# Kernel optimization log

Hardware: AMD Instinct MI355X
Metric: run time of the kernel (lower is better)

Reference implementation:

```python
import jax, jax.numpy as jnp
import numpy as np

B, IN, HS = 4096, 1024, 1024


def setup_inputs() -> dict:
    key = jax.random.key(0)
    ks = jax.random.split(key, 20)
    inp = {
        "x": jax.random.normal(ks[0], (B, IN), jnp.float32),
        "h": jax.random.normal(ks[1], (B, HS), jnp.float32),
        "c": jax.random.normal(ks[2], (B, HS), jnp.float32),
    }
    names_x = ["Wix", "Wfx", "Wgx", "Wox"]
    names_h = ["Wih", "Wfh", "Wgh", "Woh"]
    bnames_x = ["bix", "bfx", "bgx", "box"]
    bnames_h = ["bih", "bfh", "bgh", "boh"]
    k = 3
    for wn, bn in zip(names_x, bnames_x):
        inp[wn] = jax.random.normal(ks[k], (HS, IN), jnp.float32) * 0.02; k += 1
        inp[bn] = jax.random.normal(ks[k], (HS,), jnp.float32) * 0.02; k += 1
    for wn, bn in zip(names_h, bnames_h):
        inp[wn] = jax.random.normal(ks[k], (HS, HS), jnp.float32) * 0.02; k += 1
        inp[bn] = jax.random.normal(ks[k], (HS,), jnp.float32) * 0.02; k += 1
    return inp


def reference(x, h, c,
              Wix, bix, Wfx, bfx, Wgx, bgx, Wox, box,
              Wih, bih, Wfh, bfh, Wgh, bgh, Woh, boh):
    # torch Linear: y = x @ W.T + b
    i = jax.nn.sigmoid(x @ Wix.T + bix + h @ Wih.T + bih)
    f = jax.nn.sigmoid(x @ Wfx.T + bfx + h @ Wfh.T + bfh)
    g = jnp.tanh(x @ Wgx.T + bgx + h @ Wgh.T + bgh)
    o = jax.nn.sigmoid(x @ Wox.T + box + h @ Woh.T + boh)
    c_new = f * c + i * g
    h_new = o * jnp.tanh(c_new)
    return (h_new, c_new)
```

## Files before the change

kernel.cpp:

```cpp
#include <hip/hip_runtime.h>
#include <hip/hip_bf16.h>
#include <stdint.h>

#define BATCH  4096
#define IN_DIM 1024
#define HS     1024
#define K_DIM  2048
#define N_DIM  4096
#define BK 64
#define NKT (K_DIM / BK)
#define HALF_BYTES 16384
#define TPB_BYTES  (NKT * HALF_BYTES)

typedef __bf16 bf16x8 __attribute__((ext_vector_type(8)));
typedef float  f32x4  __attribute__((ext_vector_type(4)));

__device__ __forceinline__ unsigned short f2bf(float f) {
    union { float f; uint32_t u; } a; a.f = f;
    uint32_t r = a.u + 0x7FFF + ((a.u >> 16) & 1);
    return (unsigned short)(r >> 16);
}
__device__ __forceinline__ uint32_t pk2(float a, float b) {
    return (uint32_t)f2bf(a) | ((uint32_t)f2bf(b) << 16);
}

__device__ __forceinline__ void load16_lds(const void* g, void* l) {
    __builtin_amdgcn_global_load_lds(
        (const __attribute__((address_space(1))) uint32_t*)g,
        (__attribute__((address_space(3))) uint32_t*)(uintptr_t)l,
        16, 0, 0);
}
__device__ __forceinline__ void stage16k(const char* g, char* l, int wid, int lane) {
    load16_lds(g + wid * 1024 + lane * 16,        l + wid * 1024);
    load16_lds(g + 8192 + wid * 1024 + lane * 16, l + 8192 + wid * 1024);
}

__device__ __forceinline__ float sigf(float x)  { return 1.0f / (1.0f + __expf(-x)); }
__device__ __forceinline__ float tanhf_(float x){ return 1.0f - 2.0f / (__expf(2.0f * x) + 1.0f); }

#define BAR()   __builtin_amdgcn_s_barrier()
#define DSB()   __builtin_amdgcn_sched_barrier(0)
#define PRIO(x) __builtin_amdgcn_s_setprio(x)

__device__ __forceinline__ void rdA(bf16x8 (&d)[4], const char* base, int kb) {
    #pragma unroll
    for (int i = 0; i < 4; ++i) d[i] = *(const bf16x8*)(base + i * 2048 + kb);
}
__device__ __forceinline__ void rdB(bf16x8 (&d)[4], const char* base, int kb) {
    #pragma unroll
    for (int i = 0; i < 4; ++i) d[i] = *(const bf16x8*)(base + i * 2048 + kb);
}
__device__ __forceinline__ void mfma16(f32x4 (&acc)[8][4], int mh,
                                       const bf16x8 (&a)[4], const bf16x8 (&b)[4]) {
    #pragma unroll
    for (int i = 0; i < 4; ++i)
        #pragma unroll
        for (int j = 0; j < 4; ++j)
            acc[mh * 4 + i][j] = __builtin_amdgcn_mfma_f32_16x16x32_bf16(
                a[i], b[j], acc[mh * 4 + i][j], 0, 0, 0);
}

__global__ void pack_kernel(const float* __restrict__ x, const float* __restrict__ h,
                            const float* __restrict__ Wix, const float* __restrict__ Wfx,
                            const float* __restrict__ Wgx, const float* __restrict__ Wox,
                            const float* __restrict__ Wih, const float* __restrict__ Wfh,
                            const float* __restrict__ Wgh, const float* __restrict__ Woh,
                            uint4* __restrict__ Apk, uint4* __restrict__ Bpk)
{
    int t = blockIdx.x * blockDim.x + threadIdx.x;
    const int NCHUNK = (BATCH * K_DIM) / 8;
    bool isB = t >= NCHUNK;
    int ci = isB ? (t - NCHUNK) : t;

    int cb  = ci & 7;
    int row = (ci >> 3) & 127;
    int kt  = (ci >> 10) & 31;
    int bt  = ci >> 15;

    int k0 = kt * BK + ((cb ^ (row & 7)) << 3);
    int gr = bt * 128 + row;

    const float* src;
    if (!isB) {
        src = (k0 < IN_DIM) ? (x + (size_t)gr * IN_DIM + k0)
                            : (h + (size_t)gr * HS + (k0 - IN_DIM));
    } else {
        int q = (gr >> 4) & 3;
        int u = ((gr >> 6) << 4) | (gr & 15);
        const float* Wq = (k0 < IN_DIM)
            ? ((q == 0) ? Wix : (q == 1) ? Wfx : (q == 2) ? Wgx : Wox)
            : ((q == 0) ? Wih : (q == 1) ? Wfh : (q == 2) ? Wgh : Woh);
        int kk = (k0 < IN_DIM) ? k0 : (k0 - IN_DIM);
        src = Wq + (size_t)u * 1024 + kk;
    }
    float4 v0 = ((const float4*)src)[0];
    float4 v1 = ((const float4*)src)[1];
    uint4 o;
    o.x = pk2(v0.x, v0.y); o.y = pk2(v0.z, v0.w);
    o.z = pk2(v1.x, v1.y); o.w = pk2(v1.z, v1.w);
    (isB ? Bpk : Apk)[ci] = o;
}

__global__ void __launch_bounds__(512, 2)
gemm_kernel(const char* __restrict__ Apk, const char* __restrict__ Bpk,
            const float* __restrict__ c,
            const float* __restrict__ bix, const float* __restrict__ bfx,
            const float* __restrict__ bgx, const float* __restrict__ box_,
            const float* __restrict__ bih, const float* __restrict__ bfh,
            const float* __restrict__ bgh, const float* __restrict__ boh,
            float* __restrict__ out)
{
    __shared__ uint4 lds4[131072 / 16];
    char* lds = (char*)lds4;

    const int tid  = threadIdx.x;
    const int lane = tid & 63;
    const int wid  = tid >> 6;
    const int wm   = wid >> 2;
    const int wn   = wid & 3;
    const int fr   = lane & 15;
    const int kg   = lane >> 4;

    const int phys = blockIdx.x;
    const int virt = (phys & 7) * 32 + (phys >> 3);
    const int bn   = virt & 15;
    const int bm   = virt >> 4;

    const char* gA = Apk + (size_t)(bm * 2) * TPB_BYTES;
    const char* gB = Bpk + (size_t)(bn * 2) * TPB_BYTES;

    const int sw  = (fr & 7) << 4;
    const int kb0 = (kg * 16) ^ sw;
    const int kb1 = (64 + kg * 16) ^ sw;
    const int aB  = wm * HALF_BYTES + fr * 128;
    const int bB  = 32768 + (wn >> 1) * HALF_BYTES + ((wn & 1) * 64 + fr) * 128;

    f32x4 acc[8][4] = {};

    stage16k(gA + (size_t)(0 * NKT + 0) * HALF_BYTES, lds + 0,     wid, lane);
    stage16k(gA + (size_t)(1 * NKT + 0) * HALF_BYTES, lds + 16384, wid, lane);
    stage16k(gB + (size_t)(0 * NKT + 0) * HALF_BYTES, lds + 32768, wid, lane);
    stage16k(gB + (size_t)(1 * NKT + 0) * HALF_BYTES, lds + 49152, wid, lane);
    stage16k(gB + (size_t)(0 * NKT + 1) * HALF_BYTES, lds + 65536 + 32768, wid, lane);
    stage16k(gB + (size_t)(1 * NKT + 1) * HALF_BYTES, lds + 65536 + 49152, wid, lane);
    asm volatile("s_waitcnt vmcnt(4)" ::: "memory");
    BAR(); DSB();

    for (int kt = 0; kt < NKT; ++kt) {
        char* L  = lds + (kt & 1) * 65536;
        char* Ln = lds + ((kt & 1) ^ 1) * 65536;
        const bool s1 = (kt + 1 < NKT), s2 = (kt + 2 < NKT);
        bf16x8 aX[4], aY[4], b0[4], b1[4];

        rdA(aX, L + aB, kb0);
        rdB(b0, L + bB, kb0);
        if (s1) stage16k(gA + (size_t)(0 * NKT + kt + 1) * HALF_BYTES, Ln + 0, wid, lane);
        PRIO(1); mfma16(acc, 0, aX, b0); PRIO(0);
        BAR(); DSB();

        rdA(aY, L + aB, kb1);
        rdB(b1, L + bB, kb1);
        if (s1) stage16k(gA + (size_t)(1 * NKT + kt + 1) * HALF_BYTES, Ln + 16384, wid, lane);
        PRIO(1); mfma16(acc, 0, aY, b1); PRIO(0);
        BAR(); DSB();

        rdA(aX, L + aB + 8192, kb0);
        if (s2) stage16k(gB + (size_t)(0 * NKT + kt + 2) * HALF_BYTES, L + 32768, wid, lane);
        PRIO(1); mfma16(acc, 1, aX, b0); PRIO(0);
        BAR(); DSB();

        rdA(aY, L + aB + 8192, kb1);
        if (s2) stage16k(gB + (size_t)(1 * NKT + kt + 2) * HALF_BYTES, L + 49152, wid, lane);
        PRIO(1); mfma16(acc, 1, aY, b1); PRIO(0);
        if (kt < NKT - 2) asm volatile("s_waitcnt vmcnt(4)" ::: "memory");
        else              asm volatile("s_waitcnt vmcnt(0)" ::: "memory");
        BAR(); DSB();
    }

    const int u  = bn * 64 + wn * 16 + fr;
    const int r0 = bm * 256 + wm * 128;
    const float bi = bix[u] + bih[u];
    const float bf = bfx[u] + bfh[u];
    const float bg = bgx[u] + bgh[u];
    const float bo = box_[u] + boh[u];
    float* hout = out;
    float* cout = out + (size_t)BATCH * HS;

    #pragma unroll
    for (int ai = 0; ai < 8; ++ai) {
        const int rowb = r0 + ai * 16 + kg * 4;
        #pragma unroll
        for (int r = 0; r < 4; ++r) {
            const size_t idx = (size_t)(rowb + r) * HS + u;
            float iv = sigf  (acc[ai][0][r] + bi);
            float fv = sigf  (acc[ai][1][r] + bf);
            float gv = tanhf_(acc[ai][2][r] + bg);
            float ov = sigf  (acc[ai][3][r] + bo);
            float cn = fv * c[idx] + iv * gv;
            hout[idx] = ov * tanhf_(cn);
            cout[idx] = cn;
        }
    }
}

extern "C" void kernel_launch(void* const* d_in, const int* in_sizes, int n_in,
                              void* d_out, int out_size, void* d_ws, size_t ws_size,
                              hipStream_t stream)
{
    const float* x   = (const float*)d_in[0];
    const float* h   = (const float*)d_in[1];
    const float* c   = (const float*)d_in[2];
    const float* Wix = (const float*)d_in[3];  const float* bix = (const float*)d_in[4];
    const float* Wfx = (const float*)d_in[5];  const float* bfx = (const float*)d_in[6];
    const float* Wgx = (const float*)d_in[7];  const float* bgx = (const float*)d_in[8];
    const float* Wox = (const float*)d_in[9];  const float* box_ = (const float*)d_in[10];
    const float* Wih = (const float*)d_in[11]; const float* bih = (const float*)d_in[12];
    const float* Wfh = (const float*)d_in[13]; const float* bfh = (const float*)d_in[14];
    const float* Wgh = (const float*)d_in[15]; const float* bgh = (const float*)d_in[16];
    const float* Woh = (const float*)d_in[17]; const float* boh = (const float*)d_in[18];

    char* ws = (char*)d_ws;
    uint4* Apk = (uint4*)ws;
    uint4* Bpk = (uint4*)(ws + (size_t)16 * 1024 * 1024);

    pack_kernel<<<8192, 256, 0, stream>>>(x, h, Wix, Wfx, Wgx, Wox,
                                          Wih, Wfh, Wgh, Woh, Apk, Bpk);
    gemm_kernel<<<256, 512, 0, stream>>>((const char*)Apk, (const char*)Bpk, c,
                                         bix, bfx, bgx, box_, bih, bfh, bgh, boh,
                                         (float*)d_out);
}
```

Before: 84.34 us.

## Restructure GEMM main loop with register double-buffered fragments and deeper prefetch

Rewrites the K-loop of the fused LSTM GEMM so that B fragments are double-buffered in registers and A fragments are read one quarter-step ahead. Global-to-LDS staging for both A and B is now issued two tiles ahead, and the loop is unrolled by two with a single barrier per MFMA quarter. Scheduling barriers are removed and the waitcnt thresholds are retuned, so LDS read latency should overlap with MFMA work. The trade-offs are higher register pressure, a few wasted wrap-around prefetches at the end of the loop, and tighter LDS overwrite hazards that depend on the barrier placement being correct.

After: 83.51 us. Within noise of the previous version (-1.0%).

```diff
diff --git a/kernel.cpp b/kernel.cpp
--- a/kernel.cpp
+++ b/kernel.cpp
@@ -39,25 +39,32 @@
 __device__ __forceinline__ float tanhf_(float x){ return 1.0f - 2.0f / (__expf(2.0f * x) + 1.0f); }
 
 #define BAR()   __builtin_amdgcn_s_barrier()
-#define DSB()   __builtin_amdgcn_sched_barrier(0)
 #define PRIO(x) __builtin_amdgcn_s_setprio(x)
 
-__device__ __forceinline__ void rdA(bf16x8 (&d)[4], const char* base, int kb) {
+__device__ __forceinline__ void rdA4(bf16x8 (&d)[4], const char* base, int kb0, int kb1) {
+    d[0] = *(const bf16x8*)(base + kb0);
+    d[1] = *(const bf16x8*)(base + kb1);
+    d[2] = *(const bf16x8*)(base + 2048 + kb0);
+    d[3] = *(const bf16x8*)(base + 2048 + kb1);
+}
+__device__ __forceinline__ void rdB8(bf16x8 (&d)[8], const char* base, int kb0, int kb1) {
     #pragma unroll
-    for (int i = 0; i < 4; ++i) d[i] = *(const bf16x8*)(base + i * 2048 + kb);
-}
-__device__ __forceinline__ void rdB(bf16x8 (&d)[4], const char* base, int kb) {
+    for (int j = 0; j < 4; ++j) {
+        d[j]     = *(const bf16x8*)(base + j * 2048 + kb0);
+        d[4 + j] = *(const bf16x8*)(base + j * 2048 + kb1);
+    }
+}
+template<int Q>
+__device__ __forceinline__ void mfq(f32x4 (&acc)[8][4], const bf16x8 (&a)[4],
+                                    const bf16x8 (&b)[8]) {
     #pragma unroll
-    for (int i = 0; i < 4; ++i) d[i] = *(const bf16x8*)(base + i * 2048 + kb);
-}
-__device__ __forceinline__ void mfma16(f32x4 (&acc)[8][4], int mh,
-                                       const bf16x8 (&a)[4], const bf16x8 (&b)[4]) {
-    #pragma unroll
-    for (int i = 0; i < 4; ++i)
+    for (int mf = 0; mf < 2; ++mf)
         #pragma unroll
-        for (int j = 0; j < 4; ++j)
-            acc[mh * 4 + i][j] = __builtin_amdgcn_mfma_f32_16x16x32_bf16(
-                a[i], b[j], acc[mh * 4 + i][j], 0, 0, 0);
+        for (int ks = 0; ks < 2; ++ks)
+            #pragma unroll
+            for (int j = 0; j < 4; ++j)
+                acc[2 * Q + mf][j] = __builtin_amdgcn_mfma_f32_16x16x32_bf16(
+                    a[mf * 2 + ks], b[ks * 4 + j], acc[2 * Q + mf][j], 0, 0, 0);
 }
 
 __global__ void pack_kernel(const float* __restrict__ x, const float* __restrict__ h,
@@ -129,13 +136,13 @@
     const char* gA = Apk + (size_t)(bm * 2) * TPB_BYTES;
     const char* gB = Bpk + (size_t)(bn * 2) * TPB_BYTES;
 
-    const int sw  = (fr & 7) << 4;
-    const int kb0 = (kg * 16) ^ sw;
-    const int kb1 = (64 + kg * 16) ^ sw;
-    const int aB  = wm * HALF_BYTES + fr * 128;
-    const int bB  = 32768 + (wn >> 1) * HALF_BYTES + ((wn & 1) * 64 + fr) * 128;
+    const int kb0   = (kg * 16) ^ ((fr & 7) << 4);
+    const int kb1   = kb0 ^ 64;
+    const int aBase = wm * 16384 + fr * 128;
+    const int bBase = 32768 + wn * 8192 + fr * 128;
 
     f32x4 acc[8][4] = {};
+    bf16x8 aE[4], aO[4], bA_[8], bB_[8];
 
     stage16k(gA + (size_t)(0 * NKT + 0) * HALF_BYTES, lds + 0,     wid, lane);
     stage16k(gA + (size_t)(1 * NKT + 0) * HALF_BYTES, lds + 16384, wid, lane);
@@ -143,39 +150,42 @@
     stage16k(gB + (size_t)(1 * NKT + 0) * HALF_BYTES, lds + 49152, wid, lane);
     stage16k(gB + (size_t)(0 * NKT + 1) * HALF_BYTES, lds + 65536 + 32768, wid, lane);
     stage16k(gB + (size_t)(1 * NKT + 1) * HALF_BYTES, lds + 65536 + 49152, wid, lane);
-    asm volatile("s_waitcnt vmcnt(4)" ::: "memory");
-    BAR(); DSB();
-
-    for (int kt = 0; kt < NKT; ++kt) {
-        char* L  = lds + (kt & 1) * 65536;
-        char* Ln = lds + ((kt & 1) ^ 1) * 65536;
-        const bool s1 = (kt + 1 < NKT), s2 = (kt + 2 < NKT);
-        bf16x8 aX[4], aY[4], b0[4], b1[4];
-
-        rdA(aX, L + aB, kb0);
-        rdB(b0, L + bB, kb0);
-        if (s1) stage16k(gA + (size_t)(0 * NKT + kt + 1) * HALF_BYTES, Ln + 0, wid, lane);
-        PRIO(1); mfma16(acc, 0, aX, b0); PRIO(0);
-        BAR(); DSB();
-
-        rdA(aY, L + aB, kb1);
-        rdB(b1, L + bB, kb1);
-        if (s1) stage16k(gA + (size_t)(1 * NKT + kt + 1) * HALF_BYTES, Ln + 16384, wid, lane);
-        PRIO(1); mfma16(acc, 0, aY, b1); PRIO(0);
-        BAR(); DSB();
-
-        rdA(aX, L + aB + 8192, kb0);
-        if (s2) stage16k(gB + (size_t)(0 * NKT + kt + 2) * HALF_BYTES, L + 32768, wid, lane);
-        PRIO(1); mfma16(acc, 1, aX, b0); PRIO(0);
-        BAR(); DSB();
-
-        rdA(aY, L + aB + 8192, kb1);
-        if (s2) stage16k(gB + (size_t)(1 * NKT + kt + 2) * HALF_BYTES, L + 49152, wid, lane);
-        PRIO(1); mfma16(acc, 1, aY, b1); PRIO(0);
-        if (kt < NKT - 2) asm volatile("s_waitcnt vmcnt(4)" ::: "memory");
-        else              asm volatile("s_waitcnt vmcnt(0)" ::: "memory");
-        BAR(); DSB();
-    }
+    stage16k(gA + (size_t)(0 * NKT + 1) * HALF_BYTES, lds + 65536 + 0,     wid, lane);
+    stage16k(gA + (size_t)(1 * NKT + 1) * HALF_BYTES, lds + 65536 + 16384, wid, lane);
+    asm volatile("s_waitcnt vmcnt(8)" ::: "memory");
+    BAR();
+    rdB8(bA_, lds + bBase, kb0, kb1);
+    rdA4(aE, lds + aBase, kb0, kb1);
+
+#define TILE(L, LN, KT2, BCUR, BNXT)                                          \
+    {                                                                 \
+      asm volatile("s_waitcnt vmcnt(4)" ::: "memory");                        \
+      stage16k(gB + (size_t)(0 * NKT + (KT2)) * HALF_BYTES, (L) + 32768, wid, lane); \
+      rdA4(aO, (L) + aBase + 4096, kb0, kb1);                                 \
+      rdB8(BNXT, (LN) + bBase, kb0, kb1);                                     \
+      PRIO(1); mfq<0>(acc, aE, BCUR); PRIO(0); BAR();                         \
+                                                                      \
+      stage16k(gB + (size_t)(1 * NKT + (KT2)) * HALF_BYTES, (L) + 49152, wid, lane); \
+      rdA4(aE, (L) + aBase + 8192, kb0, kb1);                                 \
+      PRIO(1); mfq<1>(acc, aO, BCUR); PRIO(0); BAR();                         \
+                                                                      \
+      stage16k(gA + (size_t)(0 * NKT + (KT2)) * HALF_BYTES, (L) + 0, wid, lane); \
+      rdA4(aO, (L) + aBase + 12288, kb0, kb1);                                \
+      PRIO(1); mfq<2>(acc, aE, BCUR); PRIO(0); BAR();                         \
+                                                                      \
+      asm volatile("s_waitcnt vmcnt(6)" ::: "memory");                        \
+      stage16k(gA + (size_t)(1 * NKT + (KT2)) * HALF_BYTES, (L) + 16384, wid, lane); \
+      rdA4(aE, (LN) + aBase, kb0, kb1);                                       \
+      PRIO(1); mfq<3>(acc, aO, BCUR); PRIO(0); BAR();                         \
+    }
+
+    for (int it = 0; it < NKT / 2; ++it) {
+        const int k2e = (it * 2 + 2) & (NKT - 1);
+        const int k2o = (it * 2 + 3) & (NKT - 1);
+        TILE(lds,         lds + 65536, k2e, bA_, bB_);
+        TILE(lds + 65536, lds,         k2o, bB_, bA_);
+    }
+#undef TILE
 
     const int u  = bn * 64 + wn * 16 + fr;
     const int r0 = bm * 256 + wm * 128;
```

## Split waves into ping-pong groups with staggered LDS reads and MFMA phases

Applied to the files above, without the earlier changes.

The GEMM main loop is split by wave row: wm==0 waves read fragments then run MFMA right away, while wm==1 waves preload fragments one phase ahead, including the next k-tile's first fragments. Paired barriers offset the two groups so that one group's LDS reads and global-to-LDS staging overlap the other group's MFMA bursts. The intent is to hide LDS latency and keep the matrix cores busy. In exchange it doubles the barriers per phase and adds register pressure from prefetched fragments, and the barrier counts of the two groups must match exactly.

Result: no change. 84.38 us (+0.0%).

```diff
diff --git a/kernel.cpp b/kernel.cpp
--- a/kernel.cpp
+++ b/kernel.cpp
@@ -41,6 +41,9 @@
 #define BAR()   __builtin_amdgcn_s_barrier()
 #define DSB()   __builtin_amdgcn_sched_barrier(0)
 #define PRIO(x) __builtin_amdgcn_s_setprio(x)
+#define LGKM0() do { asm volatile("s_waitcnt lgkmcnt(0)" ::: "memory"); \
+                     __builtin_amdgcn_sched_barrier(0); } while (0)
+#define VMC(n)  asm volatile("s_waitcnt vmcnt(" #n ")" ::: "memory")
 
 __device__ __forceinline__ void rdA(bf16x8 (&d)[4], const char* base, int kb) {
     #pragma unroll
@@ -129,9 +132,8 @@
     const char* gA = Apk + (size_t)(bm * 2) * TPB_BYTES;
     const char* gB = Bpk + (size_t)(bn * 2) * TPB_BYTES;
 
-    const int sw  = (fr & 7) << 4;
-    const int kb0 = (kg * 16) ^ sw;
-    const int kb1 = (64 + kg * 16) ^ sw;
+    const int kb0 = (kg * 16) ^ ((fr & 7) << 4);
+    const int kb1 = kb0 ^ 64;
     const int aB  = wm * HALF_BYTES + fr * 128;
     const int bB  = 32768 + (wn >> 1) * HALF_BYTES + ((wn & 1) * 64 + fr) * 128;
 
@@ -143,38 +145,57 @@
     stage16k(gB + (size_t)(1 * NKT + 0) * HALF_BYTES, lds + 49152, wid, lane);
     stage16k(gB + (size_t)(0 * NKT + 1) * HALF_BYTES, lds + 65536 + 32768, wid, lane);
     stage16k(gB + (size_t)(1 * NKT + 1) * HALF_BYTES, lds + 65536 + 49152, wid, lane);
-    asm volatile("s_waitcnt vmcnt(4)" ::: "memory");
+    VMC(4);
     BAR(); DSB();
 
-    for (int kt = 0; kt < NKT; ++kt) {
-        char* L  = lds + (kt & 1) * 65536;
-        char* Ln = lds + ((kt & 1) ^ 1) * 65536;
-        const bool s1 = (kt + 1 < NKT), s2 = (kt + 2 < NKT);
-        bf16x8 aX[4], aY[4], b0[4], b1[4];
-
-        rdA(aX, L + aB, kb0);
-        rdB(b0, L + bB, kb0);
-        if (s1) stage16k(gA + (size_t)(0 * NKT + kt + 1) * HALF_BYTES, Ln + 0, wid, lane);
-        PRIO(1); mfma16(acc, 0, aX, b0); PRIO(0);
-        BAR(); DSB();
-
-        rdA(aY, L + aB, kb1);
-        rdB(b1, L + bB, kb1);
-        if (s1) stage16k(gA + (size_t)(1 * NKT + kt + 1) * HALF_BYTES, Ln + 16384, wid, lane);
-        PRIO(1); mfma16(acc, 0, aY, b1); PRIO(0);
-        BAR(); DSB();
-
-        rdA(aX, L + aB + 8192, kb0);
-        if (s2) stage16k(gB + (size_t)(0 * NKT + kt + 2) * HALF_BYTES, L + 32768, wid, lane);
-        PRIO(1); mfma16(acc, 1, aX, b0); PRIO(0);
-        BAR(); DSB();
-
-        rdA(aY, L + aB + 8192, kb1);
-        if (s2) stage16k(gB + (size_t)(1 * NKT + kt + 2) * HALF_BYTES, L + 49152, wid, lane);
-        PRIO(1); mfma16(acc, 1, aY, b1); PRIO(0);
-        if (kt < NKT - 2) asm volatile("s_waitcnt vmcnt(4)" ::: "memory");
-        else              asm volatile("s_waitcnt vmcnt(0)" ::: "memory");
-        BAR(); DSB();
+    if (wm == 0) {
+        for (int kt = 0; kt < NKT; ++kt) {
+            char* L  = lds + (kt & 1) * 65536;
+            char* Ln = lds + ((kt & 1) ^ 1) * 65536;
+            const bool s1 = (kt + 1 < NKT), s2 = (kt + 2 < NKT);
+            bf16x8 aX[4], aY[4], b0[4], b1[4];
+
+            rdA(aX, L + aB, kb0); rdB(b0, L + bB, kb0);
+            if (s1) stage16k(gA + (size_t)(0 * NKT + kt + 1) * HALF_BYTES, Ln + 0, wid, lane);
+            BAR(); LGKM0(); PRIO(1); mfma16(acc, 0, aX, b0); PRIO(0); BAR();
+            rdA(aY, L + aB, kb1); rdB(b1, L + bB, kb1);
+            if (s1) stage16k(gA + (size_t)(1 * NKT + kt + 1) * HALF_BYTES, Ln + 16384, wid, lane);
+            BAR(); LGKM0(); PRIO(1); mfma16(acc, 0, aY, b1); PRIO(0); BAR();
+            rdA(aX, L + aB + 8192, kb0);
+            if (s2) stage16k(gB + (size_t)(0 * NKT + kt + 2) * HALF_BYTES, L + 32768, wid, lane);
+            BAR(); LGKM0(); PRIO(1); mfma16(acc, 1, aX, b0); PRIO(0); BAR();
+            rdA(aY, L + aB + 8192, kb1);
+            if (s2) stage16k(gB + (size_t)(1 * NKT + kt + 2) * HALF_BYTES, L + 49152, wid, lane);
+            if (kt < NKT - 2)       VMC(4);
+            else if (kt == NKT - 2) VMC(0);
+            BAR(); LGKM0(); PRIO(1); mfma16(acc, 1, aY, b1); PRIO(0); BAR();
+        }
+    } else {
+        bf16x8 aU[4], aV[4], b0[4], b1[4];
+        rdA(aU, lds + aB, kb0);
+        rdB(b0, lds + bB, kb0);
+        for (int kt = 0; kt < NKT; ++kt) {
+            char* L  = lds + (kt & 1) * 65536;
+            char* Ln = lds + ((kt & 1) ^ 1) * 65536;
+            const bool s1 = (kt + 1 < NKT), s2 = (kt + 2 < NKT);
+
+            if (s1) stage16k(gA + (size_t)(0 * NKT + kt + 1) * HALF_BYTES, Ln + 0, wid, lane);
+            rdA(aV, L + aB, kb1); rdB(b1, L + bB, kb1);
+            BAR(); PRIO(1); mfma16(acc, 0, aU, b0); PRIO(0); BAR();
+            if (s1) stage16k(gA + (size_t)(1 * NKT + kt + 1) * HALF_BYTES, Ln + 16384, wid, lane);
+            rdA(aU, L + aB + 8192, kb0);
+            BAR(); PRIO(1); mfma16(acc, 0, aV, b1); PRIO(0); BAR();
+            if (s2) stage16k(gB + (size_t)(0 * NKT + kt + 2) * HALF_BYTES, L + 32768, wid, lane);
+            rdA(aV, L + aB + 8192, kb1);
+            BAR(); PRIO(1); mfma16(acc, 1, aU, b0); PRIO(0); BAR();
+            if (s2) stage16k(gB + (size_t)(1 * NKT + kt + 2) * HALF_BYTES, L + 49152, wid, lane);
+            if (kt < NKT - 2)       VMC(4);
+            else if (kt == NKT - 2) VMC(0);
+            BAR(); DSB();
+            asm volatile("" ::: "memory");
+            if (s1) { rdA(aU, Ln + aB, kb0); rdB(b0, Ln + bB, kb0); }
+            PRIO(1); mfma16(acc, 1, aV, b1); PRIO(0); BAR();
+        }
     }
 
     const int u  = bn * 64 + wn * 16 + fr;
```

## Shrink GEMM tile to 256x128xBK32 with triple-buffered LDS pipeline

Applied to the files above, without the earlier changes.

Changes the fused LSTM GEMM from 256x256 tiles with BK=64 and a double buffer to 256x128 tiles with BK=32 and a three-stage LDS ring, doubling the grid to 512 blocks and raising the occupancy hint. The pack kernel layout is rewritten to match the new tile shape. The epilogue prefetches the c values before the last k-step so their load latency overlaps compute. The aim is better CU coverage and occupancy. In exchange, smaller tiles reuse data less, B is reread more often from global memory, and the loop runs more iterations with a barrier in each.

New measurement: 95.04 us. 12.7% more time.

```diff
diff --git a/kernel.cpp b/kernel.cpp
--- a/kernel.cpp
+++ b/kernel.cpp
@@ -7,10 +7,13 @@
 #define HS     1024
 #define K_DIM  2048
 #define N_DIM  4096
-#define BK 64
+#define BM 256
+#define BN 128
+#define BK 32
 #define NKT (K_DIM / BK)
-#define HALF_BYTES 16384
-#define TPB_BYTES  (NKT * HALF_BYTES)
+#define A_TILE 16384
+#define B_TILE 8192
+#define BUF_BYTES (A_TILE + B_TILE)
 
 typedef __bf16 bf16x8 __attribute__((ext_vector_type(8)));
 typedef float  f32x4  __attribute__((ext_vector_type(4)));
@@ -30,10 +33,6 @@
         (__attribute__((address_space(3))) uint32_t*)(uintptr_t)l,
         16, 0, 0);
 }
-__device__ __forceinline__ void stage16k(const char* g, char* l, int wid, int lane) {
-    load16_lds(g + wid * 1024 + lane * 16,        l + wid * 1024);
-    load16_lds(g + 8192 + wid * 1024 + lane * 16, l + 8192 + wid * 1024);
-}
 
 __device__ __forceinline__ float sigf(float x)  { return 1.0f / (1.0f + __expf(-x)); }
 __device__ __forceinline__ float tanhf_(float x){ return 1.0f - 2.0f / (__expf(2.0f * x) + 1.0f); }
@@ -41,24 +40,7 @@
 #define BAR()   __builtin_amdgcn_s_barrier()
 #define DSB()   __builtin_amdgcn_sched_barrier(0)
 #define PRIO(x) __builtin_amdgcn_s_setprio(x)
-
-__device__ __forceinline__ void rdA(bf16x8 (&d)[4], const char* base, int kb) {
-    #pragma unroll
-    for (int i = 0; i < 4; ++i) d[i] = *(const bf16x8*)(base + i * 2048 + kb);
-}
-__device__ __forceinline__ void rdB(bf16x8 (&d)[4], const char* base, int kb) {
-    #pragma unroll
-    for (int i = 0; i < 4; ++i) d[i] = *(const bf16x8*)(base + i * 2048 + kb);
-}
-__device__ __forceinline__ void mfma16(f32x4 (&acc)[8][4], int mh,
-                                       const bf16x8 (&a)[4], const bf16x8 (&b)[4]) {
-    #pragma unroll
-    for (int i = 0; i < 4; ++i)
-        #pragma unroll
-        for (int j = 0; j < 4; ++j)
-            acc[mh * 4 + i][j] = __builtin_amdgcn_mfma_f32_16x16x32_bf16(
-                a[i], b[j], acc[mh * 4 + i][j], 0, 0, 0);
-}
+#define VMC(n)  asm volatile("s_waitcnt vmcnt(" #n ")" ::: "memory")
 
 __global__ void pack_kernel(const float* __restrict__ x, const float* __restrict__ h,
                             const float* __restrict__ Wix, const float* __restrict__ Wfx,
@@ -72,21 +54,27 @@
     bool isB = t >= NCHUNK;
     int ci = isB ? (t - NCHUNK) : t;
 
-    int cb  = ci & 7;
-    int row = (ci >> 3) & 127;
-    int kt  = (ci >> 10) & 31;
-    int bt  = ci >> 15;
-
-    int k0 = kt * BK + ((cb ^ (row & 7)) << 3);
-    int gr = bt * 128 + row;
-
     const float* src;
     if (!isB) {
-        src = (k0 < IN_DIM) ? (x + (size_t)gr * IN_DIM + k0)
-                            : (h + (size_t)gr * HS + (k0 - IN_DIM));
+        int cb = ci & 7;
+        int lr = (ci >> 3) & 127;
+        int kt = (ci >> 10) & 63;
+        int bt = ci >> 16;
+        int sc = cb ^ (lr & 7);
+        int m  = bt * 256 + ((sc >> 2) << 7) + lr;
+        int k0 = kt * 32 + (sc & 3) * 8;
+        src = (k0 < IN_DIM) ? (x + (size_t)m * IN_DIM + k0)
+                            : (h + (size_t)m * HS + (k0 - IN_DIM));
     } else {
-        int q = (gr >> 4) & 3;
-        int u = ((gr >> 6) << 4) | (gr & 15);
+        int cb = ci & 7;
+        int lr = (ci >> 3) & 63;
+        int kt = (ci >> 9) & 63;
+        int bt = ci >> 15;
+        int sc = cb ^ (lr & 7);
+        int np = bt * 128 + ((sc >> 2) << 6) + lr;
+        int k0 = kt * 32 + (sc & 3) * 8;
+        int q  = (np >> 4) & 3;
+        int u  = ((np >> 6) << 4) | (np & 15);
         const float* Wq = (k0 < IN_DIM)
             ? ((q == 0) ? Wix : (q == 1) ? Wfx : (q == 2) ? Wgx : Wox)
             : ((q == 0) ? Wih : (q == 1) ? Wfh : (q == 2) ? Wgh : Woh);
@@ -101,7 +89,7 @@
     (isB ? Bpk : Apk)[ci] = o;
 }
 
-__global__ void __launch_bounds__(512, 2)
+__global__ void __launch_bounds__(512, 4)
 gemm_kernel(const char* __restrict__ Apk, const char* __restrict__ Bpk,
             const float* __restrict__ c,
             const float* __restrict__ bix, const float* __restrict__ bfx,
@@ -110,95 +98,145 @@
             const float* __restrict__ bgh, const float* __restrict__ boh,
             float* __restrict__ out)
 {
-    __shared__ uint4 lds4[131072 / 16];
+    __shared__ uint4 lds4[(3 * BUF_BYTES) / 16];
     char* lds = (char*)lds4;
 
     const int tid  = threadIdx.x;
     const int lane = tid & 63;
     const int wid  = tid >> 6;
-    const int wm   = wid >> 2;
-    const int wn   = wid & 3;
+    const int wm   = wid >> 1;
+    const int wn   = wid & 1;
     const int fr   = lane & 15;
     const int kg   = lane >> 4;
 
     const int phys = blockIdx.x;
-    const int virt = (phys & 7) * 32 + (phys >> 3);
-    const int bn   = virt & 15;
-    const int bm   = virt >> 4;
-
-    const char* gA = Apk + (size_t)(bm * 2) * TPB_BYTES;
-    const char* gB = Bpk + (size_t)(bn * 2) * TPB_BYTES;
-
-    const int sw  = (fr & 7) << 4;
-    const int kb0 = (kg * 16) ^ sw;
-    const int kb1 = (64 + kg * 16) ^ sw;
-    const int aB  = wm * HALF_BYTES + fr * 128;
-    const int bB  = 32768 + (wn >> 1) * HALF_BYTES + ((wn & 1) * 64 + fr) * 128;
-
-    f32x4 acc[8][4] = {};
-
-    stage16k(gA + (size_t)(0 * NKT + 0) * HALF_BYTES, lds + 0,     wid, lane);
-    stage16k(gA + (size_t)(1 * NKT + 0) * HALF_BYTES, lds + 16384, wid, lane);
-    stage16k(gB + (size_t)(0 * NKT + 0) * HALF_BYTES, lds + 32768, wid, lane);
-    stage16k(gB + (size_t)(1 * NKT + 0) * HALF_BYTES, lds + 49152, wid, lane);
-    stage16k(gB + (size_t)(0 * NKT + 1) * HALF_BYTES, lds + 65536 + 32768, wid, lane);
-    stage16k(gB + (size_t)(1 * NKT + 1) * HALF_BYTES, lds + 65536 + 49152, wid, lane);
-    asm volatile("s_waitcnt vmcnt(4)" ::: "memory");
-    BAR(); DSB();
-
-    for (int kt = 0; kt < NKT; ++kt) {
-        char* L  = lds + (kt & 1) * 65536;
-        char* Ln = lds + ((kt & 1) ^ 1) * 65536;
-        const bool s1 = (kt + 1 < NKT), s2 = (kt + 2 < NKT);
-        bf16x8 aX[4], aY[4], b0[4], b1[4];
-
-        rdA(aX, L + aB, kb0);
-        rdB(b0, L + bB, kb0);
-        if (s1) stage16k(gA + (size_t)(0 * NKT + kt + 1) * HALF_BYTES, Ln + 0, wid, lane);
-        PRIO(1); mfma16(acc, 0, aX, b0); PRIO(0);
-        BAR(); DSB();
-
-        rdA(aY, L + aB, kb1);
-        rdB(b1, L + bB, kb1);
-        if (s1) stage16k(gA + (size_t)(1 * NKT + kt + 1) * HALF_BYTES, Ln + 16384, wid, lane);
-        PRIO(1); mfma16(acc, 0, aY, b1); PRIO(0);
-        BAR(); DSB();
-
-        rdA(aX, L + aB + 8192, kb0);
-        if (s2) stage16k(gB + (size_t)(0 * NKT + kt + 2) * HALF_BYTES, L + 32768, wid, lane);
-        PRIO(1); mfma16(acc, 1, aX, b0); PRIO(0);
-        BAR(); DSB();
-
-        rdA(aY, L + aB + 8192, kb1);
-        if (s2) stage16k(gB + (size_t)(1 * NKT + kt + 2) * HALF_BYTES, L + 49152, wid, lane);
-        PRIO(1); mfma16(acc, 1, aY, b1); PRIO(0);
-        if (kt < NKT - 2) asm volatile("s_waitcnt vmcnt(4)" ::: "memory");
-        else              asm volatile("s_waitcnt vmcnt(0)" ::: "memory");
-        BAR(); DSB();
+    const int virt = (phys & 7) * 64 + (phys >> 3);
+    const int bn   = virt & 31;
+    const int bm   = virt >> 5;
+
+    const char* gAp = Apk + (size_t)bm * (NKT * A_TILE);
+    const char* gBp = Bpk + (size_t)bn * (NKT * B_TILE);
+    const char* gAs = gAp + tid * 16;
+    const char* gBs = gBp + tid * 16;
+
+    const int swz   = (fr & 7) << 4;
+    const int aBase = (((wm & 1) * 64 + fr) * 128) + ((((wm >> 1) << 6) + kg * 16) ^ swz);
+    const int bBase = A_TILE + fr * 128 + (((wn << 6) + kg * 16) ^ swz);
+
+    f32x4 acc[4][4] = {};
+    bf16x8 a0, a1, a2, a3, b0, b1, b2, b3;
+
+    char* Lc  = lds;
+    char* Ln1 = lds + BUF_BYTES;
+    char* Ln2 = lds + 2 * BUF_BYTES;
+
+    load16_lds(gAs,                 Lc + tid * 16);
+    load16_lds(gAs + 8192,          Lc + 8192 + tid * 16);
+    load16_lds(gBs,                 Lc + A_TILE + tid * 16);
+    load16_lds(gAs + A_TILE,        Ln1 + tid * 16);
+    load16_lds(gAs + A_TILE + 8192, Ln1 + 8192 + tid * 16);
+    load16_lds(gBs + B_TILE,        Ln1 + A_TILE + tid * 16);
+    VMC(3);
+    BAR();
+
+    for (int t = 0; t < NKT - 1; ++t) {
+        if (t + 2 < NKT) {
+            load16_lds(gAs + (size_t)(t + 2) * A_TILE,        Ln2 + tid * 16);
+            load16_lds(gAs + (size_t)(t + 2) * A_TILE + 8192, Ln2 + 8192 + tid * 16);
+            load16_lds(gBs + (size_t)(t + 2) * B_TILE,        Ln2 + A_TILE + tid * 16);
+        }
+        a0 = *(const bf16x8*)(Lc + aBase);
+        a1 = *(const bf16x8*)(Lc + aBase + 2048);
+        a2 = *(const bf16x8*)(Lc + aBase + 4096);
+        a3 = *(const bf16x8*)(Lc + aBase + 6144);
+        b0 = *(const bf16x8*)(Lc + bBase);
+        b1 = *(const bf16x8*)(Lc + bBase + 2048);
+        b2 = *(const bf16x8*)(Lc + bBase + 4096);
+        b3 = *(const bf16x8*)(Lc + bBase + 6144);
+        PRIO(1);
+        acc[0][0] = __builtin_amdgcn_mfma_f32_16x16x32_bf16(a0, b0, acc[0][0], 0, 0, 0);
+        acc[0][1] = __builtin_amdgcn_mfma_f32_16x16x32_bf16(a0, b1, acc[0][1], 0, 0, 0);
+        acc[0][2] = __builtin_amdgcn_mfma_f32_16x16x32_bf16(a0, b2, acc[0][2], 0, 0, 0);
+        acc[0][3] = __builtin_amdgcn_mfma_f32_16x16x32_bf16(a0, b3, acc[0][3], 0, 0, 0);
+        acc[1][0] = __builtin_amdgcn_mfma_f32_16x16x32_bf16(a1, b0, acc[1][0], 0, 0, 0);
+        acc[1][1] = __builtin_amdgcn_mfma_f32_16x16x32_bf16(a1, b1, acc[1][1], 0, 0, 0);
+        acc[1][2] = __builtin_amdgcn_mfma_f32_16x16x32_bf16(a1, b2, acc[1][2], 0, 0, 0);
+        acc[1][3] = __builtin_amdgcn_mfma_f32_16x16x32_bf16(a1, b3, acc[1][3], 0, 0, 0);
+        acc[2][0] = __builtin_amdgcn_mfma_f32_16x16x32_bf16(a2, b0, acc[2][0], 0, 0, 0);
+        acc[2][1] = __builtin_amdgcn_mfma_f32_16x16x32_bf16(a2, b1, acc[2][1], 0, 0, 0);
+        acc[2][2] = __builtin_amdgcn_mfma_f32_16x16x32_bf16(a2, b2, acc[2][2], 0, 0, 0);
+        acc[2][3] = __builtin_amdgcn_mfma_f32_16x16x32_bf16(a2, b3, acc[2][3], 0, 0, 0);
+        acc[3][0] = __builtin_amdgcn_mfma_f32_16x16x32_bf16(a3, b0, acc[3][0], 0, 0, 0);
+        acc[3][1] = __builtin_amdgcn_mfma_f32_16x16x32_bf16(a3, b1, acc[3][1], 0, 0, 0);
+        acc[3][2] = __builtin_amdgcn_mfma_f32_16x16x32_bf16(a3, b2, acc[3][2], 0, 0, 0);
+        acc[3][3] = __builtin_amdgcn_mfma_f32_16x16x32_bf16(a3, b3, acc[3][3], 0, 0, 0);
+        PRIO(0);
+        DSB();
+        if (t < NKT - 2) VMC(3);
+        else             VMC(0);
+        BAR();
+        char* tmp = Lc; Lc = Ln1; Ln1 = Ln2; Ln2 = tmp;
     }
 
-    const int u  = bn * 64 + wn * 16 + fr;
-    const int r0 = bm * 256 + wm * 128;
-    const float bi = bix[u] + bih[u];
-    const float bf = bfx[u] + bfh[u];
-    const float bg = bgx[u] + bgh[u];
-    const float bo = box_[u] + boh[u];
-    float* hout = out;
-    float* cout = out + (size_t)BATCH * HS;
-
-    #pragma unroll
-    for (int ai = 0; ai < 8; ++ai) {
-        const int rowb = r0 + ai * 16 + kg * 4;
+    const int u  = (bn * 2 + wn) * 16 + fr;
+    const int r0 = bm * 256 + wm * 64;
+    {
+        float cpre[4][4];
         #pragma unroll
-        for (int r = 0; r < 4; ++r) {
-            const size_t idx = (size_t)(rowb + r) * HS + u;
-            float iv = sigf  (acc[ai][0][r] + bi);
-            float fv = sigf  (acc[ai][1][r] + bf);
-            float gv = tanhf_(acc[ai][2][r] + bg);
-            float ov = sigf  (acc[ai][3][r] + bo);
-            float cn = fv * c[idx] + iv * gv;
-            hout[idx] = ov * tanhf_(cn);
-            cout[idx] = cn;
+        for (int i = 0; i < 4; ++i) {
+            const int rowb = r0 + i * 16 + kg * 4;
+            #pragma unroll
+            for (int r = 0; r < 4; ++r)
+                cpre[i][r] = c[(size_t)(rowb + r) * HS + u];
+        }
+        const float bi = bix[u] + bih[u];
+        const float bf = bfx[u] + bfh[u];
+        const float bg = bgx[u] + bgh[u];
+        const float bo = box_[u] + boh[u];
+
+        a0 = *(const bf16x8*)(Lc + aBase);
+        a1 = *(const bf16x8*)(Lc + aBase + 2048);
+        a2 = *(const bf16x8*)(Lc + aBase + 4096);
+        a3 = *(const bf16x8*)(Lc + aBase + 6144);
+        b0 = *(const bf16x8*)(Lc + bBase);
+        b1 = *(const bf16x8*)(Lc + bBase + 2048);
+        b2 = *(const bf16x8*)(Lc + bBase + 4096);
+        b3 = *(const bf16x8*)(Lc + bBase + 6144);
+        PRIO(1);
+        acc[0][0] = __builtin_amdgcn_mfma_f32_16x16x32_bf16(a0, b0, acc[0][0], 0, 0, 0);
+        acc[0][1] = __builtin_amdgcn_mfma_f32_16x16x32_bf16(a0, b1, acc[0][1], 0, 0, 0);
+        acc[0][2] = __builtin_amdgcn_mfma_f32_16x16x32_bf16(a0, b2, acc[0][2], 0, 0, 0);
+        acc[0][3] = __builtin_amdgcn_mfma_f32_16x16x32_bf16(a0, b3, acc[0][3], 0, 0, 0);
+        acc[1][0] = __builtin_amdgcn_mfma_f32_16x16x32_bf16(a1, b0, acc[1][0], 0, 0, 0);
+        acc[1][1] = __builtin_amdgcn_mfma_f32_16x16x32_bf16(a1, b1, acc[1][1], 0, 0, 0);
+        acc[1][2] = __builtin_amdgcn_mfma_f32_16x16x32_bf16(a1, b2, acc[1][2], 0, 0, 0);
+        acc[1][3] = __builtin_amdgcn_mfma_f32_16x16x32_bf16(a1, b3, acc[1][3], 0, 0, 0);
+        acc[2][0] = __builtin_amdgcn_mfma_f32_16x16x32_bf16(a2, b0, acc[2][0], 0, 0, 0);
+        acc[2][1] = __builtin_amdgcn_mfma_f32_16x16x32_bf16(a2, b1, acc[2][1], 0, 0, 0);
+        acc[2][2] = __builtin_amdgcn_mfma_f32_16x16x32_bf16(a2, b2, acc[2][2], 0, 0, 0);
+        acc[2][3] = __builtin_amdgcn_mfma_f32_16x16x32_bf16(a2, b3, acc[2][3], 0, 0, 0);
+        acc[3][0] = __builtin_amdgcn_mfma_f32_16x16x32_bf16(a3, b0, acc[3][0], 0, 0, 0);
+        acc[3][1] = __builtin_amdgcn_mfma_f32_16x16x32_bf16(a3, b1, acc[3][1], 0, 0, 0);
+        acc[3][2] = __builtin_amdgcn_mfma_f32_16x16x32_bf16(a3, b2, acc[3][2], 0, 0, 0);
+        acc[3][3] = __builtin_amdgcn_mfma_f32_16x16x32_bf16(a3, b3, acc[3][3], 0, 0, 0);
+        PRIO(0);
+
+        float* hout = out;
+        float* cout = out + (size_t)BATCH * HS;
+        #pragma unroll
+        for (int i = 0; i < 4; ++i) {
+            const int rowb = r0 + i * 16 + kg * 4;
+            #pragma unroll
+            for (int r = 0; r < 4; ++r) {
+                const size_t idx = (size_t)(rowb + r) * HS + u;
+                float iv = sigf  (acc[i][0][r] + bi);
+                float fv = sigf  (acc[i][1][r] + bf);
+                float gv = tanhf_(acc[i][2][r] + bg);
+                float ov = sigf  (acc[i][3][r] + bo);
+                float cn = fv * cpre[i][r] + iv * gv;
+                hout[idx] = ov * tanhf_(cn);
+                cout[idx] = cn;
+            }
         }
     }
 }
@@ -225,7 +263,7 @@
 
     pack_kernel<<<8192, 256, 0, stream>>>(x, h, Wix, Wfx, Wgx, Wox,
                                           Wih, Wfh, Wgh, Woh, Apk, Bpk);
-    gemm_kernel<<<256, 512, 0, stream>>>((const char*)Apk, (const char*)Bpk, c,
+    gemm_kernel<<<512, 512, 0, stream>>>((const char*)Apk, (const char*)Bpk, c,
                                          bix, bfx, bgx, box_, bih, bfh, bgh, boh,
                                          (float*)d_out);
 }
```
